# Kernel tuning notes

Measured on AMD Instinct MI355X. Metric: run time of the kernel, lower is better.

Reference implementation:

```python
import jax, jax.numpy as jnp
import numpy as np

EMBED_DIM = 1024
NUM_HEADS = 16
D_K = EMBED_DIM // NUM_HEADS


def setup_inputs() -> dict:
    key = jax.random.key(0)
    ks = jax.random.split(key, 5)
    x = jax.random.normal(ks[0], (2, 2048, EMBED_DIM), dtype=jnp.float32)
    # kaiming_normal on 2D params: std = sqrt(2/fan_in) with fan_in = in_features
    w_qkv = jax.random.normal(ks[1], (3 * EMBED_DIM, EMBED_DIM), dtype=jnp.float32) * np.sqrt(2.0 / EMBED_DIM)
    b_qkv = jnp.zeros((3 * EMBED_DIM,), dtype=jnp.float32)
    w_o = jax.random.normal(ks[2], (EMBED_DIM, EMBED_DIM), dtype=jnp.float32) * np.sqrt(2.0 / EMBED_DIM)
    b_o = jnp.zeros((EMBED_DIM,), dtype=jnp.float32)
    return {"x": x, "w_qkv": w_qkv, "b_qkv": b_qkv, "w_o": w_o, "b_o": b_o}


def reference(x, w_qkv, b_qkv, w_o, b_o):
    B, N, C = x.shape
    qkv = x @ w_qkv.T + b_qkv  # [B,N,3C]
    q, k, v = jnp.split(qkv, 3, axis=-1)
    # [B,H,N,d_k]
    q = q.reshape(B, N, NUM_HEADS, D_K).transpose(0, 2, 1, 3)
    k = k.reshape(B, N, NUM_HEADS, D_K).transpose(0, 2, 1, 3)
    v = v.reshape(B, N, NUM_HEADS, D_K).transpose(0, 2, 1, 3)
    # NOTE: original forward scales by 1/sqrt(embed_dim), not 1/sqrt(d_k)
    scores = jnp.einsum('bhqd,bhkd->bhqk', q, k) / np.sqrt(C).astype(np.float32)
    causal = jnp.tril(jnp.ones((N, N), dtype=bool))
    scores = jnp.where(causal, scores, -jnp.inf)
    attn = jax.nn.softmax(scores, axis=-1)
    out = jnp.einsum('bhqk,bhkd->bhqd', attn, v)  # [B,H,N,d_k]
    out = out.transpose(0, 2, 1, 3).reshape(B, N, C)
    return out @ w_o.T + b_o
```

## Files before the change

### kernel.cpp

```cpp
#include <hip/hip_runtime.h>
#include <hip/hip_bf16.h>
#include <math.h>

typedef __bf16 bf16_t;
typedef __bf16 bf16x8 __attribute__((ext_vector_type(8)));
typedef __bf16 bf16x4 __attribute__((ext_vector_type(4)));
typedef __bf16 bf16x2 __attribute__((ext_vector_type(2)));
typedef float f32x4 __attribute__((ext_vector_type(4)));

#define SCALE_L2E 0.045084234f

#define MFMA16(a, b, c) __builtin_amdgcn_mfma_f32_16x16x32_bf16(a, b, c, 0, 0, 0)

__global__ void convert3_f32_bf16(const float* __restrict__ a, int na,
                                  const float* __restrict__ b, int nb,
                                  const float* __restrict__ c, int nc,
                                  bf16_t* __restrict__ oa, bf16_t* __restrict__ ob,
                                  bf16_t* __restrict__ oc) {
  int i = (blockIdx.x * blockDim.x + threadIdx.x) * 8;
  const float* src;
  bf16_t* dst;
  int off;
  if (i < na) { src = a; dst = oa; off = i; }
  else if (i < na + nb) { src = b; dst = ob; off = i - na; }
  else if (i < na + nb + nc) { src = c; dst = oc; off = i - na - nb; }
  else return;
  float4 u = *(const float4*)&src[off];
  float4 v = *(const float4*)&src[off + 4];
  bf16x8 w = {(bf16_t)u.x, (bf16_t)u.y, (bf16_t)u.z, (bf16_t)u.w,
              (bf16_t)v.x, (bf16_t)v.y, (bf16_t)v.z, (bf16_t)v.w};
  *(bf16x8*)&dst[off] = w;
}

#define GLOBAL_AS __attribute__((address_space(1)))
#define LDS_AS __attribute__((address_space(3)))
__device__ __forceinline__ void g2l16(const void* g, void* l) {
  __builtin_amdgcn_global_load_lds((const GLOBAL_AS void*)g, (LDS_AS void*)l,
                                   16, 0, 0);
}

template <typename TC, int BN>
__launch_bounds__(256)
__global__ void gemm_bt_bias(const bf16_t* __restrict__ A,
                             const bf16_t* __restrict__ B,
                             const float* __restrict__ bias,
                             TC* __restrict__ C,
                             int M, int N, int K) {
  constexpr int NT = BN / 32;
  __shared__ bf16_t As[128 * 32];
  __shared__ bf16_t Bs[BN * 32];

  const int t = threadIdx.x;
  const int wave = t >> 6, lane = t & 63, quad = lane >> 4, ln = lane & 15;
  const int wm = (wave >> 1) * 64, wn = (wave & 1) * (BN / 2);
  const int m0 = blockIdx.y * 128, n0 = blockIdx.x * BN;

  const int srow = lane >> 2;
  const int schunk = ((lane & 3) ^ ((lane >> 3) & 3)) * 8;
  const bf16_t* gA0 = &A[(size_t)(m0 + wave * 32 + srow) * K + schunk];
  const bf16_t* gA1 = gA0 + (size_t)16 * K;
  bf16_t* lA0 = &As[(wave * 32) * 32];
  bf16_t* lA1 = &As[(wave * 32 + 16) * 32];
  const bf16_t* gB0 = &B[(size_t)(n0 + (BN == 128 ? wave * 32 : wave * 16) + srow) * K + schunk];
  const bf16_t* gB1 = gB0 + (size_t)16 * K;
  bf16_t* lB0 = &Bs[((BN == 128 ? wave * 32 : wave * 16)) * 32];
  bf16_t* lB1 = &Bs[(wave * 32 + 16) * 32];

  const int cslot = (quad ^ ((ln >> 1) & 3)) * 8;

  f32x4 acc[4][NT];
  for (int i = 0; i < 4; i++)
    for (int j = 0; j < NT; j++) acc[i][j] = (f32x4){0.f, 0.f, 0.f, 0.f};

  for (int k0 = 0; k0 < K; k0 += 32) {
    __syncthreads();
    g2l16(gA0 + k0, lA0);
    g2l16(gA1 + k0, lA1);
    g2l16(gB0 + k0, lB0);
    if (BN == 128) g2l16(gB1 + k0, lB1);
    __syncthreads();

    bf16x8 af[4], bfr[NT];
    for (int mt = 0; mt < 4; mt++)
      af[mt] = *(const bf16x8*)&As[(wm + mt * 16 + ln) * 32 + cslot];
    for (int nt = 0; nt < NT; nt++)
      bfr[nt] = *(const bf16x8*)&Bs[(wn + nt * 16 + ln) * 32 + cslot];
    for (int mt = 0; mt < 4; mt++)
      for (int nt = 0; nt < NT; nt++)
        acc[mt][nt] = MFMA16(af[mt], bfr[nt], acc[mt][nt]);
  }

  for (int nt = 0; nt < NT; nt++) {
    int col = n0 + wn + nt * 16 + ln;
    float bv = bias[col];
    for (int mt = 0; mt < 4; mt++) {
      int row = m0 + wm + mt * 16 + quad * 4;
      for (int r = 0; r < 4; r++)
        C[(size_t)(row + r) * N + col] = (TC)(acc[mt][nt][r] + bv);
    }
  }
}

__launch_bounds__(256, 2)
__global__ void attn_kernel(const bf16_t* __restrict__ qkv,
                            bf16_t* __restrict__ out) {
  constexpr int KP = 72, VP = 72;
  __shared__ __align__(16) bf16_t Ks[64 * KP];
  __shared__ __align__(16) bf16_t Vt[64 * VP];

  const int t = threadIdx.x;
  const int wave = t >> 6, lane = t & 63, quad = lane >> 4, ln = lane & 15;
  const int p = blockIdx.x & 15;
  const int bh = blockIdx.x >> 4;
  const int b = bh >> 4, h = bh & 15;
  const int qA = p * 64, qB = (31 - p) * 64;
  const int itA = p + 1, ntiles = 32 - p;
  const size_t rs = 3072;
  const size_t base = (size_t)b * 2048 * rs;

  const size_t qoffA = base + (size_t)(qA + wave * 16 + ln) * rs + h * 64;
  const size_t qoffB = base + (size_t)(qB + wave * 16 + ln) * rs + h * 64;
  bf16x8 qfA0 = *(const bf16x8*)&qkv[qoffA + quad * 8];
  bf16x8 qfA1 = *(const bf16x8*)&qkv[qoffA + 32 + quad * 8];
  bf16x8 qfB0 = *(const bf16x8*)&qkv[qoffB + quad * 8];
  bf16x8 qfB1 = *(const bf16x8*)&qkv[qoffB + 32 + quad * 8];

  f32x4 oA[4], oB[4];
  float lAx = 0.f, lBx = 0.f;
  for (int ct = 0; ct < 4; ct++) {
    oA[ct] = (f32x4){0.f, 0.f, 0.f, 0.f};
    oB[ct] = (f32x4){0.f, 0.f, 0.f, 0.f};
  }

  const int r0 = t >> 3, c0 = (t & 7) * 8;
  const bf16_t* Kg = &qkv[base + 1024 + h * 64];
  const bf16_t* Vg = &qkv[base + 2048 + h * 64];
  const int ksA = r0 * KP + (((t & 7) + wave) & 7) * 8;
  const int ksB = (r0 + 32) * KP + (((t & 7) + wave + 4) & 7) * 8;
  const int vkoff = ((((r0 >> 2) + (t & 7)) & 7)) * 8 + 2 * (r0 & 3);

  bf16x8 ka = *(const bf16x8*)&Kg[(size_t)r0 * rs + c0];
  bf16x8 kb = *(const bf16x8*)&Kg[(size_t)(r0 + 32) * rs + c0];
  bf16x8 va2 = *(const bf16x8*)&Vg[(size_t)(2 * r0) * rs + c0];
  bf16x8 vb2 = *(const bf16x8*)&Vg[(size_t)(2 * r0 + 1) * rs + c0];

  const int qgA = qA + wave * 16 + ln;
  const int qgB = qB + wave * 16 + ln;

  for (int kt = 0; kt < ntiles; kt++) {
    __syncthreads();
    *(bf16x8*)&Ks[ksA] = ka;
    *(bf16x8*)&Ks[ksB] = kb;
#pragma unroll
    for (int j = 0; j < 8; j++) {
      bf16x2 w2 = {va2[j], vb2[j]};
      *(bf16x2*)&Vt[(c0 + j) * VP + vkoff] = w2;
    }
    __syncthreads();

    if (kt + 1 < ntiles) {
      const size_t nb_ = (size_t)(kt + 1) * 64;
      ka = *(const bf16x8*)&Kg[(nb_ + r0) * rs + c0];
      kb = *(const bf16x8*)&Kg[(nb_ + r0 + 32) * rs + c0];
      va2 = *(const bf16x8*)&Vg[(nb_ + 2 * r0) * rs + c0];
      vb2 = *(const bf16x8*)&Vg[(nb_ + 2 * r0 + 1) * rs + c0];
    }

    const bool doA = (kt < itA);
    const bool dgA = (kt == itA - 1);
    const bool dgB = (kt == ntiles - 1);
    const int kbase = kt * 64;

    bf16x8 BpA[4], BpB[4];
#pragma unroll
    for (int st = 0; st < 4; st++) {
      const int krow = st * 16 + ln;
      const int rot = 2 * st + (ln >> 3);
      bf16x8 kf0 = *(const bf16x8*)&Ks[krow * KP + ((quad + rot) & 7) * 8];
      bf16x8 kf1 = *(const bf16x8*)&Ks[krow * KP + ((quad + 4 + rot) & 7) * 8];
      const int k0g = kbase + st * 16 + quad * 4;
      if (doA) {
        f32x4 s = (f32x4){0.f, 0.f, 0.f, 0.f};
        s = MFMA16(kf0, qfA0, s);
        s = MFMA16(kf1, qfA1, s);
        bf16x8 f = (bf16x8){0, 0, 0, 0, 0, 0, 0, 0};
#pragma unroll
        for (int r = 0; r < 4; r++) {
          float pv = exp2f(s[r] * SCALE_L2E);
          if (dgA && (k0g + r > qgA)) pv = 0.f;
          lAx += pv;
          f[r] = (bf16_t)pv;
        }
        BpA[st] = f;
      }
      {
        f32x4 s = (f32x4){0.f, 0.f, 0.f, 0.f};
        s = MFMA16(kf0, qfB0, s);
        s = MFMA16(kf1, qfB1, s);
        bf16x8 f = (bf16x8){0, 0, 0, 0, 0, 0, 0, 0};
#pragma unroll
        for (int r = 0; r < 4; r++) {
          float pv = exp2f(s[r] * SCALE_L2E);
          if (dgB && (k0g + r > qgB)) pv = 0.f;
          lBx += pv;
          f[r] = (bf16_t)pv;
        }
        BpB[st] = f;
      }
    }

#pragma unroll
    for (int st = 0; st < 4; st++) {
#pragma unroll
      for (int ct = 0; ct < 4; ct++) {
        const int d = ct * 16 + ln;
        const int C = (2 * st + (quad >> 1) + 2 * ct + (ln >> 3)) & 7;
        bf16x4 v4 = *(const bf16x4*)&Vt[d * VP + C * 8 + (quad & 1) * 4];
        bf16x8 A8 = {v4[0], v4[1], v4[2], v4[3], 0, 0, 0, 0};
        if (doA) oA[ct] = MFMA16(A8, BpA[st], oA[ct]);
        oB[ct] = MFMA16(A8, BpB[st], oB[ct]);
      }
    }
  }

  lAx += __shfl_xor(lAx, 16);
  lAx += __shfl_xor(lAx, 32);
  lBx += __shfl_xor(lBx, 16);
  lBx += __shfl_xor(lBx, 32);
  const float invA = 1.0f / lAx, invB = 1.0f / lBx;
  const int ocol = h * 64 + quad * 4;
#pragma unroll
  for (int ct = 0; ct < 4; ct++) {
    bf16x4 wa, wb;
#pragma unroll
    for (int r = 0; r < 4; r++) {
      wa[r] = (bf16_t)(oA[ct][r] * invA);
      wb[r] = (bf16_t)(oB[ct][r] * invB);
    }
    *(bf16x4*)&out[(size_t)(b * 2048 + qgA) * 1024 + ocol + ct * 16] = wa;
    *(bf16x4*)&out[(size_t)(b * 2048 + qgB) * 1024 + ocol + ct * 16] = wb;
  }
}

extern "C" void kernel_launch(void* const* d_in, const int* in_sizes, int n_in,
                              void* d_out, int out_size, void* d_ws, size_t ws_size,
                              hipStream_t stream) {
  const float* x     = (const float*)d_in[0];
  const float* w_qkv = (const float*)d_in[1];
  const float* b_qkv = (const float*)d_in[2];
  const float* w_o   = (const float*)d_in[3];
  const float* b_o   = (const float*)d_in[4];
  float* out = (float*)d_out;

  bf16_t* qkv   = (bf16_t*)d_ws;
  bf16_t* xbf   = qkv + (size_t)4096 * 3072;
  bf16_t* wqkvb = xbf + (size_t)4096 * 1024;
  bf16_t* wob   = wqkvb + (size_t)3072 * 1024;
  bf16_t* attn  = xbf;

  const int na = 4096 * 1024, nb = 3072 * 1024, nc = 1024 * 1024;
  convert3_f32_bf16<<<dim3((na + nb + nc) / (256 * 8)), 256, 0, stream>>>(
      x, na, w_qkv, nb, w_o, nc, xbf, wqkvb, wob);

  gemm_bt_bias<bf16_t, 128><<<dim3(3072 / 128, 4096 / 128), 256, 0, stream>>>(
      xbf, wqkvb, b_qkv, qkv, 4096, 3072, 1024);
  attn_kernel<<<dim3(512), 256, 0, stream>>>(qkv, attn);
  gemm_bt_bias<float, 64><<<dim3(1024 / 64, 4096 / 128), 256, 0, stream>>>(
      attn, wob, b_o, out, 4096, 1024, 1024);
}
```

Measured before the change: 209.1 us.

## Pack two key subtiles per PV MFMA and use fast exp2/rcp with truncating bf16 pack

The PV product previously fed half-zero 8-wide operands to the 16x16x32 MFMA. It now packs the probabilities of two 16-key subtiles into one full bf16x8 operand and gathers the matching two V chunks, which halves the PV MFMA count. The exp path uses the raw hardware exp2 with a fused bias that compensates for truncation, and it packs to bf16 by byte-permute truncation instead of rounding conversion. The final normalisation uses the hardware reciprocal. These trade a small loss of numerical accuracy for fewer instructions.

```diff
diff --git a/kernel.cpp b/kernel.cpp
--- a/kernel.cpp
+++ b/kernel.cpp
@@ -7,10 +7,17 @@
 typedef __bf16 bf16x4 __attribute__((ext_vector_type(4)));
 typedef __bf16 bf16x2 __attribute__((ext_vector_type(2)));
 typedef float f32x4 __attribute__((ext_vector_type(4)));
+typedef unsigned u32x4 __attribute__((ext_vector_type(4)));
 
 #define SCALE_L2E 0.045084234f
+#define ROUND_B 0.0028169f
 
 #define MFMA16(a, b, c) __builtin_amdgcn_mfma_f32_16x16x32_bf16(a, b, c, 0, 0, 0)
+
+__device__ __forceinline__ unsigned pack2(float a, float b) {
+  return __builtin_amdgcn_perm(__builtin_bit_cast(unsigned, b),
+                               __builtin_bit_cast(unsigned, a), 0x07060302u);
+}
 
 __global__ void convert3_f32_bf16(const float* __restrict__ a, int na,
                                   const float* __restrict__ b, int nb,
@@ -171,54 +178,66 @@
     const bool dgB = (kt == ntiles - 1);
     const int kbase = kt * 64;
 
-    bf16x8 BpA[4], BpB[4];
-#pragma unroll
-    for (int st = 0; st < 4; st++) {
-      const int krow = st * 16 + ln;
-      const int rot = 2 * st + (ln >> 3);
-      bf16x8 kf0 = *(const bf16x8*)&Ks[krow * KP + ((quad + rot) & 7) * 8];
-      bf16x8 kf1 = *(const bf16x8*)&Ks[krow * KP + ((quad + 4 + rot) & 7) * 8];
-      const int k0g = kbase + st * 16 + quad * 4;
-      if (doA) {
-        f32x4 s = (f32x4){0.f, 0.f, 0.f, 0.f};
-        s = MFMA16(kf0, qfA0, s);
-        s = MFMA16(kf1, qfA1, s);
-        bf16x8 f = (bf16x8){0, 0, 0, 0, 0, 0, 0, 0};
-#pragma unroll
-        for (int r = 0; r < 4; r++) {
-          float pv = exp2f(s[r] * SCALE_L2E);
-          if (dgA && (k0g + r > qgA)) pv = 0.f;
-          lAx += pv;
-          f[r] = (bf16_t)pv;
+    bf16x8 BpA[2], BpB[2];
+#pragma unroll
+    for (int pr = 0; pr < 2; pr++) {
+      u32x4 uA, uB;
+#pragma unroll
+      for (int sh = 0; sh < 2; sh++) {
+        const int st = pr * 2 + sh;
+        const int krow = st * 16 + ln;
+        const int rot = 2 * st + (ln >> 3);
+        bf16x8 kf0 = *(const bf16x8*)&Ks[krow * KP + ((quad + rot) & 7) * 8];
+        bf16x8 kf1 = *(const bf16x8*)&Ks[krow * KP + ((quad + 4 + rot) & 7) * 8];
+        const int k0g = kbase + st * 16 + quad * 4;
+        if (doA) {
+          f32x4 s = (f32x4){0.f, 0.f, 0.f, 0.f};
+          s = MFMA16(kf0, qfA0, s);
+          s = MFMA16(kf1, qfA1, s);
+          float pv[4];
+#pragma unroll
+          for (int r = 0; r < 4; r++) {
+            float e = __builtin_amdgcn_exp2f(fmaf(s[r], SCALE_L2E, ROUND_B));
+            if (dgA && (k0g + r > qgA)) e = 0.f;
+            lAx += e;
+            pv[r] = e;
+          }
+          uA[sh * 2]     = pack2(pv[0], pv[1]);
+          uA[sh * 2 + 1] = pack2(pv[2], pv[3]);
         }
-        BpA[st] = f;
+        {
+          f32x4 s = (f32x4){0.f, 0.f, 0.f, 0.f};
+          s = MFMA16(kf0, qfB0, s);
+          s = MFMA16(kf1, qfB1, s);
+          float pv[4];
+#pragma unroll
+          for (int r = 0; r < 4; r++) {
+            float e = __builtin_amdgcn_exp2f(fmaf(s[r], SCALE_L2E, ROUND_B));
+            if (dgB && (k0g + r > qgB)) e = 0.f;
+            lBx += e;
+            pv[r] = e;
+          }
+          uB[sh * 2]     = pack2(pv[0], pv[1]);
+          uB[sh * 2 + 1] = pack2(pv[2], pv[3]);
+        }
       }
-      {
-        f32x4 s = (f32x4){0.f, 0.f, 0.f, 0.f};
-        s = MFMA16(kf0, qfB0, s);
-        s = MFMA16(kf1, qfB1, s);
-        bf16x8 f = (bf16x8){0, 0, 0, 0, 0, 0, 0, 0};
-#pragma unroll
-        for (int r = 0; r < 4; r++) {
-          float pv = exp2f(s[r] * SCALE_L2E);
-          if (dgB && (k0g + r > qgB)) pv = 0.f;
-          lBx += pv;
-          f[r] = (bf16_t)pv;
-        }
-        BpB[st] = f;
-      }
-    }
-
-#pragma unroll
-    for (int st = 0; st < 4; st++) {
+      BpA[pr] = __builtin_bit_cast(bf16x8, uA);
+      BpB[pr] = __builtin_bit_cast(bf16x8, uB);
+    }
+
+#pragma unroll
+    for (int pr = 0; pr < 2; pr++) {
 #pragma unroll
       for (int ct = 0; ct < 4; ct++) {
-        const int d = ct * 16 + ln;
-        const int C = (2 * st + (quad >> 1) + 2 * ct + (ln >> 3)) & 7;
-        bf16x4 v4 = *(const bf16x4*)&Vt[d * VP + C * 8 + (quad & 1) * 4];
-        bf16x8 A8 = {v4[0], v4[1], v4[2], v4[3], 0, 0, 0, 0};
-        if (doA) oA[ct] = MFMA16(A8, BpA[st], oA[ct]);
-        oB[ct] = MFMA16(A8, BpB[st], oB[ct]);
+        const int dd = ct * 16 + ln;
+        const int bc = (quad >> 1) + 2 * ct + (ln >> 3);
+        const int cA = (4 * pr + bc) & 7;
+        const int cB = (4 * pr + 2 + bc) & 7;
+        bf16x4 v0 = *(const bf16x4*)&Vt[dd * VP + cA * 8 + (quad & 1) * 4];
+        bf16x4 v1 = *(const bf16x4*)&Vt[dd * VP + cB * 8 + (quad & 1) * 4];
+        bf16x8 A8 = __builtin_shufflevector(v0, v1, 0, 1, 2, 3, 4, 5, 6, 7);
+        if (doA) oA[ct] = MFMA16(A8, BpA[pr], oA[ct]);
+        oB[ct] = MFMA16(A8, BpB[pr], oB[ct]);
       }
     }
   }
@@ -227,7 +246,8 @@
   lAx += __shfl_xor(lAx, 32);
   lBx += __shfl_xor(lBx, 16);
   lBx += __shfl_xor(lBx, 32);
-  const float invA = 1.0f / lAx, invB = 1.0f / lBx;
+  const float invA = __builtin_amdgcn_rcpf(lAx);
+  const float invB = __builtin_amdgcn_rcpf(lBx);
   const int ocol = h * 64 + quad * 4;
 #pragma unroll
   for (int ct = 0; ct < 4; ct++) {
```

Result: faster. 188.2 us (-10.0%).
